# Optimization experiments

Hardware: AMD Instinct MI355X
Metric: run time of the kernel (lower is better)

## Reference

```python
import jax, jax.numpy as jnp
import numpy as np

WIN, SHIFT = 8, 4
DIM, HEADS, MLP_H = 96, 6, 384
B, H, W = 1, 512, 512
HEAD_D = DIM // HEADS
N = WIN * WIN
EPS = 1e-5


def _rel_pos_index():
    ch = np.arange(WIN)
    coords = np.stack(np.meshgrid(ch, ch, indexing='ij')).reshape(2, -1)  # [2, 64]
    rel = (coords[:, :, None] - coords[:, None, :]).transpose(1, 2, 0)    # [64, 64, 2]
    rel[:, :, 0] += WIN - 1
    rel[:, :, 1] += WIN - 1
    rel[:, :, 0] *= 2 * WIN - 1
    return rel.sum(-1)


def _attn_mask():
    img = np.zeros((H, W))
    cnt = 0
    for hs in (slice(0, -WIN), slice(-WIN, -SHIFT), slice(-SHIFT, None)):
        for ws in (slice(0, -WIN), slice(-WIN, -SHIFT), slice(-SHIFT, None)):
            img[hs, ws] = cnt
            cnt += 1
    mw = img.reshape(H // WIN, WIN, W // WIN, WIN).transpose(0, 2, 1, 3).reshape(-1, N)
    diff = mw[:, None, :] - mw[:, :, None]
    return np.where(diff != 0, -100.0, 0.0).astype(np.float32)  # [nW, 64, 64]


REL_IDX = jnp.asarray(_rel_pos_index())
ATTN_MASK = jnp.asarray(_attn_mask())


def layernorm(x, w, b):
    mu = jnp.mean(x, axis=-1, keepdims=True)
    var = jnp.mean(jnp.square(x - mu), axis=-1, keepdims=True)
    return (x - mu) * jax.lax.rsqrt(var + EPS) * w + b


def setup_inputs() -> dict:
    key = jax.random.key(0)
    ks = jax.random.split(key, 16)
    s = 0.02
    return {
        'x': jax.random.normal(ks[0], (B, DIM, H, W), jnp.float32),
        'norm1_w': jnp.ones((DIM,), jnp.float32),
        'norm1_b': jnp.zeros((DIM,), jnp.float32),
        'qkv_w': jax.random.normal(ks[1], (3 * DIM, DIM), jnp.float32) * s,
        'qkv_b': jnp.zeros((3 * DIM,), jnp.float32),
        'rpb': jax.random.normal(ks[2], ((2 * WIN - 1) ** 2, HEADS), jnp.float32) * s,
        'proj_w': jax.random.normal(ks[3], (DIM, DIM), jnp.float32) * s,
        'proj_b': jnp.zeros((DIM,), jnp.float32),
        'norm2_w': jnp.ones((DIM,), jnp.float32),
        'norm2_b': jnp.zeros((DIM,), jnp.float32),
        'fc1_w': jax.random.normal(ks[4], (MLP_H, DIM), jnp.float32) * s,
        'fc1_b': jnp.zeros((MLP_H,), jnp.float32),
        'fc2_w': jax.random.normal(ks[5], (DIM, MLP_H), jnp.float32) * s,
        'fc2_b': jnp.zeros((DIM,), jnp.float32),
    }


def reference(x, norm1_w, norm1_b, qkv_w, qkv_b, rpb, proj_w, proj_b,
              norm2_w, norm2_b, fc1_w, fc1_b, fc2_w, fc2_b):
    nH, nW_ = H // WIN, W // WIN
    nWin = nH * nW_
    shortcut = jnp.transpose(x, (0, 2, 3, 1))            # [B,H,W,C]
    xn = layernorm(shortcut, norm1_w, norm1_b)
    xs = jnp.roll(xn, (-SHIFT, -SHIFT), axis=(1, 2))     # cyclic shift
    # window partition -> [B*nWin, N, C]
    win = xs.reshape(B, nH, WIN, nW_, WIN, DIM).transpose(0, 1, 3, 2, 4, 5)
    win = win.reshape(B * nWin, N, DIM)
    qkv = win @ qkv_w.T + qkv_b                          # [Bw, N, 3C]
    qkv = qkv.reshape(-1, N, 3, HEADS, HEAD_D).transpose(2, 0, 3, 1, 4)
    q, k, v = qkv[0], qkv[1], qkv[2]                     # [Bw, h, N, d]
    scale = HEAD_D ** -0.5
    attn = jnp.einsum('bhnd,bhmd->bhnm', q * scale, k)   # [Bw, h, 64, 64]
    bias = rpb[REL_IDX.reshape(-1)].reshape(N, N, HEADS).transpose(2, 0, 1)
    attn = attn + bias[None]
    attn = attn.reshape(B, nWin, HEADS, N, N) + ATTN_MASK[None, :, None]
    attn = jax.nn.softmax(attn.reshape(-1, HEADS, N, N), axis=-1)
    out = jnp.einsum('bhnm,bhmd->bhnd', attn, v).transpose(0, 2, 1, 3).reshape(-1, N, DIM)
    out = out @ proj_w.T + proj_b
    # window reverse + un-shift
    out = out.reshape(B, nH, nW_, WIN, WIN, DIM).transpose(0, 1, 3, 2, 4, 5).reshape(B, H, W, DIM)
    out = jnp.roll(out, (SHIFT, SHIFT), axis=(1, 2))
    x1 = shortcut + out
    h = layernorm(x1, norm2_w, norm2_b)
    h = jax.nn.gelu(h @ fc1_w.T + fc1_b, approximate=False) @ fc2_w.T + fc2_b
    x2 = x1 + h
    return jnp.transpose(x2, (0, 3, 1, 2))               # [B,C,H,W]
```

## Files before the change

kernel.cpp:

```cpp
#include <hip/hip_runtime.h>
#include <math.h>

#define WINSZ  8
#define SHIFTV 4
#define DIM    96
#define HEADS  6
#define HEAD_D 16
#define MLP_H  384
#define HH     512
#define WWID   512
#define HWSZ   (HH*WWID)
#define NTOK   64
#define EPSV   1e-5f
#define XP     97
#define QP     17
#define BFP    120

#define OFF_W1   0
#define OFF_W2   36864
#define OFF_QKV  73728
#define OFF_PROJ 101376
#define OFF_BIAS 110592
#define WS_FULL  208896
#define WS_MLP   73728

#define QKP 104
#define VTP 72
#define X1P 97
#define WBP 104

#define WBUF_OFF 38144
#define SMEM_SZ  48128

typedef __attribute__((ext_vector_type(2))) short  s2v;
typedef __attribute__((ext_vector_type(4))) short  s4v;
typedef __attribute__((ext_vector_type(8))) short  s8v;
typedef __attribute__((ext_vector_type(4))) float  f4v;
typedef __attribute__((ext_vector_type(4))) unsigned short u4v;

__device__ __forceinline__ unsigned short f2bf(float v) {
    union { float f; unsigned u; } c; c.f = v;
    unsigned r = c.u + 0x7fffu + ((c.u >> 16) & 1u);
    return (unsigned short)(r >> 16);
}
__device__ __forceinline__ float bf2f(unsigned short u) {
    union { unsigned u; float f; } c; c.u = ((unsigned)u) << 16; return c.f;
}
__device__ __forceinline__ unsigned long long shfl64(unsigned long long v, int src) {
    union { unsigned long long q; int i[2]; } c; c.q = v;
    c.i[0] = __shfl(c.i[0], src);
    c.i[1] = __shfl(c.i[1], src);
    return c.q;
}
__device__ __forceinline__ float fast_gelu(float h) {
    float h2 = h*h;
    float u  = fmaf(0.044715f, h2, 1.0f);
    float e  = __expf(-1.5957691216057308f * h * u);
    return h * __builtin_amdgcn_rcpf(1.0f + e);
}

__device__ __forceinline__ void gld_lds16(const void* g, void* l) {
    __builtin_amdgcn_global_load_lds(
        (const __attribute__((address_space(1))) unsigned*)(g),
        (__attribute__((address_space(3))) unsigned*)(l),
        16, 0, 0);
}

__device__ __forceinline__ void stage48(const char* gb, int stride_b,
                                        char* wb, int tid) {
    #pragma unroll
    for (int k = 0; k < 3; ++k) {
        int idx = tid + k*256;
        if (k < 2 || idx < 624) {
            int r   = idx / 13;
            int rem = idx - r*13;
            const char* src = (rem < 12) ? (gb + r*stride_b + rem*16) : gb;
            char* dst = wb + ((tid & ~63) + k*256)*16;
            gld_lds16(src, dst);
        }
    }
}

__global__ __launch_bounds__(256) void conv_all(
    const float* __restrict__ qkvw, const float* __restrict__ projw,
    const float* __restrict__ f1w,  const float* __restrict__ f2w,
    const float* __restrict__ rpb,  short* __restrict__ ws)
{
    int i = blockIdx.x*256 + threadIdx.x;
    if (i < 36864)        ws[OFF_W1 + i] = (short)f2bf(f1w[i]);
    else if (i < 73728)   ws[OFF_W2 + i-36864] = (short)f2bf(f2w[i-36864]);
    else if (i < 101376)  ws[OFF_QKV + i-73728] = (short)f2bf(qkvw[i-73728]);
    else if (i < 110592)  ws[OFF_PROJ + i-101376] = (short)f2bf(projw[i-101376]);
    else if (i < WS_FULL) {
        int idx = i - 110592;
        int tb = idx / 24576;
        int rm = idx - tb*24576;
        int hd = rm >> 12;
        int rc = rm & 4095;
        int r = rc >> 6, c = rc & 63;
        int rti = r>>3, rtj = r&7, cti = c>>3, ctj = c&7;
        int rel = (rti-cti+7)*15 + (rtj-ctj+7);
        float b = rpb[rel*HEADS + hd];
        int bh = tb>>1, bw = tb&1;
        int rhr = bh ? (rti<4?1:2) : 0, rhc = bh ? (cti<4?1:2) : 0;
        int rwr = bw ? (rtj<4?1:2) : 0, rwc = bw ? (ctj<4?1:2) : 0;
        if (rhr != rhc || rwr != rwc) b -= 100.f;
        ws[OFF_BIAS + idx] = (short)f2bf(b);
    }
}

__global__ __launch_bounds__(256,3) void fused_kernel(
    const float* __restrict__ x,
    const float* __restrict__ n1w, const float* __restrict__ n1b,
    const float* __restrict__ qkvb, const float* __restrict__ projb,
    const float* __restrict__ n2w, const float* __restrict__ n2b,
    const float* __restrict__ f1b, const float* __restrict__ f2b,
    const short* __restrict__ wqkv, const short* __restrict__ wproj,
    const short* __restrict__ w1b, const short* __restrict__ w2b,
    const short* __restrict__ btab,
    float* __restrict__ out)
{
    __shared__ __align__(16) char smem[SMEM_SZ];
    short* qb   = (short*)smem;
    short* kb2  = (short*)(smem + 13312);
    short* vT   = (short*)(smem + 26624);
    short* aob  = qb;
    float* x1f  = (float*)(smem + 13312);
    short* lnb2 = (short*)smem;
    short* hid  = (short*)smem;
    short* wbS  = (short*)(smem + WBUF_OFF);
    char*  wbC  = (char*)(smem + WBUF_OFF);

    const int tid  = threadIdx.x;
    const int wv   = tid >> 6, lane = tid & 63;
    const int col  = lane & 15, kq = lane >> 4;
    const int trow = wv*16 + col;

    int bid = blockIdx.x;
    int wl = (bid & 7)*512 + ((bid >> 5) << 2) + ((bid >> 3) & 3);
    const int wi = wl >> 6, wj = wl & 63;

    const int ti = trow>>3, tj = trow&7;
    const int hpos = (wi*8 + ti + SHIFTV) & (HH-1);
    const int wpos = (wj*8 + tj + SHIFTV) & (WWID-1);
    const int p = hpos*WWID + wpos;

    s8v bfr[3];
    {
        float v[24], s1 = 0.f, s2 = 0.f;
        #pragma unroll
        for (int kb = 0; kb < 3; ++kb)
            #pragma unroll
            for (int j = 0; j < 8; ++j) {
                float vv = x[(kb*32 + kq*8 + j)*HWSZ + p];
                v[kb*8+j] = vv; s1 += vv; s2 += vv*vv;
            }
        s1 += __shfl_xor(s1, 16); s2 += __shfl_xor(s2, 16);
        s1 += __shfl_xor(s1, 32); s2 += __shfl_xor(s2, 32);
        float mu = s1*(1.f/96.f);
        float rs = rsqrtf(s2*(1.f/96.f) - mu*mu + EPSV);
        #pragma unroll
        for (int kb = 0; kb < 3; ++kb) {
            f4v wA = *(const f4v*)&n1w[kb*32 + kq*8];
            f4v wB = *(const f4v*)&n1w[kb*32 + kq*8 + 4];
            f4v bA = *(const f4v*)&n1b[kb*32 + kq*8];
            f4v bB = *(const f4v*)&n1b[kb*32 + kq*8 + 4];
            s8v o;
            #pragma unroll
            for (int j = 0; j < 4; ++j) {
                o[j]   = (short)f2bf((v[kb*8+j]  -mu)*rs*wA[j] + bA[j]);
                o[4+j] = (short)f2bf((v[kb*8+4+j]-mu)*rs*wB[j] + bB[j]);
            }
            bfr[kb] = o;
        }
    }

    float shc[24];
    #pragma unroll
    for (int mt = 0; mt < 6; ++mt)
        #pragma unroll
        for (int i = 0; i < 4; ++i)
            shc[mt*4+i] = x[(mt*16 + kq*4 + i)*HWSZ + p];

    const s8v zfrag = {0,0,0,0,0,0,0,0};

    {
        #pragma unroll
        for (int g = 0; g < 6; ++g) {
            s8v aw[9];
            #pragma unroll
            for (int m = 0; m < 3; ++m)
                #pragma unroll
                for (int kb = 0; kb < 3; ++kb)
                    aw[m*3+kb] = *(const s8v*)&wqkv[((g*3+m)*16+col)*96 + kb*32 + kq*8];
            #pragma unroll
            for (int m = 0; m < 3; ++m) {
                int mt = g*3 + m;
                f4v acc = {0.f,0.f,0.f,0.f};
                #pragma unroll
                for (int kb = 0; kb < 3; ++kb)
                    acc = __builtin_amdgcn_mfma_f32_16x16x32_bf16(aw[m*3+kb], bfr[kb], acc, 0,0,0);
                int od0 = mt*16 + kq*4;
                f4v bia = *(const f4v*)&qkvb[od0];
                if (mt < 6) {
                    s4v o;
                    #pragma unroll
                    for (int i = 0; i < 4; ++i) o[i] = (short)f2bf((acc[i]+bia[i])*0.25f);
                    *(s4v*)&qb[trow*QKP + od0] = o;
                } else if (mt < 12) {
                    s4v o;
                    #pragma unroll
                    for (int i = 0; i < 4; ++i) o[i] = (short)f2bf(acc[i]+bia[i]);
                    *(s4v*)&kb2[trow*QKP + od0 - 96] = o;
                } else {
                    int d0 = od0 - 192;
                    #pragma unroll
                    for (int i = 0; i < 4; ++i)
                        vT[(d0+i)*VTP + trow] = (short)f2bf(acc[i]+bia[i]);
                }
            }
        }
    }
    __syncthreads();

    const int tb = ((wi==63)?2:0) | ((wj==63)?1:0);
    u4v bt[4];
    {
        const short* gb = btab + ((tb*6+0)<<12) + (trow<<6);
        #pragma unroll
        for (int mt = 0; mt < 4; ++mt) bt[mt] = *(const u4v*)&gb[mt*16 + kq*4];
    }
    for (int hd = 0; hd < 6; ++hd) {
        u4v btn[4];
        if (hd < 5) {
            const short* gb = btab + ((tb*6+hd+1)<<12) + (trow<<6);
            #pragma unroll
            for (int mt = 0; mt < 4; ++mt) btn[mt] = *(const u4v*)&gb[mt*16 + kq*4];
        }
        s8v bq = zfrag;
        if (kq < 2) bq = *(const s8v*)&qb[trow*QKP + hd*16 + kq*8];
        f4v st[4];
        #pragma unroll
        for (int mt = 0; mt < 4; ++mt) {
            s8v a = zfrag;
            if (kq < 2) a = *(const s8v*)&kb2[(mt*16+col)*QKP + hd*16 + kq*8];
            f4v z = {0.f,0.f,0.f,0.f};
            st[mt] = __builtin_amdgcn_mfma_f32_16x16x32_bf16(a, bq, z, 0,0,0);
        }
        float sc[16];
        #pragma unroll
        for (int mt = 0; mt < 4; ++mt) {
            #pragma unroll
            for (int i = 0; i < 4; ++i) sc[mt*4+i] = st[mt][i] + bf2f(bt[mt][i]);
        }
        float m8[8];
        #pragma unroll
        for (int j = 0; j < 8; ++j) m8[j] = fmaxf(sc[2*j], sc[2*j+1]);
        #pragma unroll
        for (int j = 0; j < 4; ++j) m8[j] = fmaxf(m8[j], m8[j+4]);
        float m = fmaxf(fmaxf(m8[0], m8[2]), fmaxf(m8[1], m8[3]));
        m = fmaxf(m, __shfl_xor(m, 16));
        m = fmaxf(m, __shfl_xor(m, 32));
        float s8r[8];
        #pragma unroll
        for (int j = 0; j < 8; ++j) {
            sc[2*j]   = __expf(sc[2*j]  -m);
            sc[2*j+1] = __expf(sc[2*j+1]-m);
            s8r[j] = sc[2*j] + sc[2*j+1];
        }
        #pragma unroll
        for (int j = 0; j < 4; ++j) s8r[j] += s8r[j+4];
        float sum = (s8r[0]+s8r[2]) + (s8r[1]+s8r[3]);
        sum += __shfl_xor(sum, 16);
        sum += __shfl_xor(sum, 32);
        unsigned long long p64[4];
        #pragma unroll
        for (int mt = 0; mt < 4; ++mt) {
            union { s4v v; unsigned long long q; } pk;
            #pragma unroll
            for (int i = 0; i < 4; ++i) pk.v[i] = (short)f2bf(sc[mt*4+i]);
            p64[mt] = pk.q;
        }
        const int s0 = col + ((kq & 1) << 5);
        const int sel = kq >> 1;
        f4v g = {0.f,0.f,0.f,0.f};
        #pragma unroll
        for (int c = 0; c < 2; ++c) {
            unsigned long long t0 = shfl64(p64[2*c],   s0);
            unsigned long long t1 = shfl64(p64[2*c+1], s0);
            unsigned long long lo = sel ? t1 : t0;
            unsigned long long u0 = shfl64(p64[2*c],   s0+16);
            unsigned long long u1 = shfl64(p64[2*c+1], s0+16);
            unsigned long long hi = sel ? u1 : u0;
            union { unsigned long long q[2]; s8v v; } bb;
            bb.q[0] = lo; bb.q[1] = hi;
            s8v a = *(const s8v*)&vT[(hd*16+col)*VTP + c*32 + kq*8];
            g = __builtin_amdgcn_mfma_f32_16x16x32_bf16(a, bb.v, g, 0,0,0);
        }
        float linv = 1.f/sum;
        s4v o;
        #pragma unroll
        for (int i = 0; i < 4; ++i) o[i] = (short)f2bf(g[i]*linv);
        *(s4v*)&aob[trow*QKP + hd*16 + kq*4] = o;
        #pragma unroll
        for (int mt = 0; mt < 4; ++mt) bt[mt] = btn[mt];
    }
    __syncthreads();

    stage48((const char*)w1b, 192, wbC, tid);

    {
        s8v bfr2[3];
        #pragma unroll
        for (int kb = 0; kb < 3; ++kb)
            bfr2[kb] = *(const s8v*)&aob[trow*QKP + kb*32 + kq*8];
        #pragma unroll
        for (int g = 0; g < 2; ++g) {
            s8v aw[9];
            #pragma unroll
            for (int m = 0; m < 3; ++m)
                #pragma unroll
                for (int kb = 0; kb < 3; ++kb)
                    aw[m*3+kb] = *(const s8v*)&wproj[((g*3+m)*16+col)*96 + kb*32 + kq*8];
            #pragma unroll
            for (int m = 0; m < 3; ++m) {
                int mt = g*3 + m;
                f4v acc = {0.f,0.f,0.f,0.f};
                #pragma unroll
                for (int kb = 0; kb < 3; ++kb)
                    acc = __builtin_amdgcn_mfma_f32_16x16x32_bf16(aw[m*3+kb], bfr2[kb], acc, 0,0,0);
                int c0 = mt*16 + kq*4;
                f4v pb4 = *(const f4v*)&projb[c0];
                #pragma unroll
                for (int i = 0; i < 4; ++i)
                    x1f[trow*X1P + c0 + i] = shc[mt*4+i] + acc[i] + pb4[i];
            }
        }
    }
    __threadfence_block();

    const int mrow = wv*16;

    {
        int t2 = mrow + col;
        float vv[24], s1 = 0.f, s2 = 0.f;
        #pragma unroll
        for (int i = 0; i < 24; ++i) {
            float v = x1f[t2*X1P + kq*24 + i]; vv[i] = v; s1 += v; s2 += v*v;
        }
        s1 += __shfl_xor(s1, 16); s2 += __shfl_xor(s2, 16);
        s1 += __shfl_xor(s1, 32); s2 += __shfl_xor(s2, 32);
        float mu = s1*(1.f/96.f);
        float rs = rsqrtf(s2*(1.f/96.f) - mu*mu + EPSV);
        #pragma unroll
        for (int i = 0; i < 12; ++i) {
            int c = kq*24 + i*2;
            s2v o;
            o[0] = (short)f2bf((vv[i*2]  -mu)*rs*n2w[c]   + n2b[c]);
            o[1] = (short)f2bf((vv[i*2+1]-mu)*rs*n2w[c+1] + n2b[c+1]);
            *(s2v*)&lnb2[t2*QKP + c] = o;
        }
    }
    __threadfence_block();

    s8v a1[3];
    #pragma unroll
    for (int kb = 0; kb < 3; ++kb)
        a1[kb] = *(const s8v*)&lnb2[(mrow+col)*QKP + kb*32 + kq*8];

    f4v acc2[6];
    #pragma unroll
    for (int n = 0; n < 6; ++n) acc2[n] = (f4v){0.f,0.f,0.f,0.f};

    __syncthreads();

    for (int ch = 0; ch < 4; ++ch) {
        const char* w1c = (const char*)w1b + ch*96*192;
        const char* w2c = (const char*)w2b + ch*192;
        #pragma unroll
        for (int half = 0; half < 2; ++half) {
            #pragma unroll
            for (int nl = 0; nl < 3; ++nl) {
                f4v acc = (f4v){0.f,0.f,0.f,0.f};
                #pragma unroll
                for (int kb = 0; kb < 3; ++kb) {
                    s8v b = *(const s8v*)&wbS[(nl*16+col)*WBP + kb*32 + kq*8];
                    acc = __builtin_amdgcn_mfma_f32_16x16x32_bf16(a1[kb], b, acc, 0,0,0);
                }
                int c = half*48 + nl*16 + col;
                float bias = f1b[ch*96 + c];
                #pragma unroll
                for (int i = 0; i < 4; ++i)
                    hid[(mrow + kq*4 + i)*QKP + c] = (short)f2bf(fast_gelu(acc[i]+bias));
            }
            __syncthreads();
            if (half == 0) stage48(w1c + 48*192, 192, wbC, tid);
            else           stage48(w2c, 768, wbC, tid);
            __syncthreads();
        }
        s8v a2[3];
        #pragma unroll
        for (int kb = 0; kb < 3; ++kb)
            a2[kb] = *(const s8v*)&hid[(mrow+col)*QKP + kb*32 + kq*8];
        #pragma unroll
        for (int half = 0; half < 2; ++half) {
            #pragma unroll
            for (int nl = 0; nl < 3; ++nl) {
                #pragma unroll
                for (int kb = 0; kb < 3; ++kb) {
                    s8v b = *(const s8v*)&wbS[(nl*16+col)*WBP + kb*32 + kq*8];
                    acc2[half*3+nl] = __builtin_amdgcn_mfma_f32_16x16x32_bf16(a2[kb], b, acc2[half*3+nl], 0,0,0);
                }
            }
            __syncthreads();
            if (half == 0)      stage48(w2c + 48*768, 768, wbC, tid);
            else if (ch < 3)    stage48((const char*)w1b + (ch+1)*96*192, 192, wbC, tid);
            __syncthreads();
        }
    }

    #pragma unroll
    for (int nt = 0; nt < 6; ++nt) {
        int c = nt*16 + col;
        float bias = f2b[c];
        #pragma unroll
        for (int i = 0; i < 4; ++i) {
            int t = mrow + kq*4 + i;
            x1f[t*X1P + c] += acc2[nt][i] + bias;
        }
    }
    __threadfence_block();
    {
        int tt = mrow + col;
        int tti = tt>>3, ttj = tt&7;
        int pp = ((wi*8 + tti + SHIFTV) & (HH-1))*WWID + ((wj*8 + ttj + SHIFTV) & (WWID-1));
        #pragma unroll
        for (int it = 0; it < 24; ++it) {
            int c = it*4 + kq;
            out[c*HWSZ + pp] = x1f[tt*X1P + c];
        }
    }
}

__global__ __launch_bounds__(256) void attn_kernel(
    const float* __restrict__ x,
    const float* __restrict__ n1w, const float* __restrict__ n1b,
    const float* __restrict__ qkvw, const float* __restrict__ qkvb,
    const float* __restrict__ rpb,
    const float* __restrict__ projw, const float* __restrict__ projb,
    float* __restrict__ out)
{
    __shared__ float xn[NTOK*XP];
    __shared__ float ao[NTOK*XP];
    __shared__ float qh[NTOK*QP];
    __shared__ float kh[NTOK*QP];
    __shared__ float vh[NTOK*QP];
    __shared__ int   srid[NTOK];
    __shared__ int   spos[NTOK];

    const int tid = threadIdx.x;
    const int blk = blockIdx.x;
    const int wi = blk >> 6, wj = blk & 63;

    {
        int t  = tid >> 2;
        int j4 = tid & 3;
        int ti = t >> 3, tj = t & 7;
        int a = wi*WINSZ + ti;
        int bcol = wj*WINSZ + tj;
        int h = (a + SHIFTV) & (HH-1);
        int w = (bcol + SHIFTV) & (WWID-1);
        int p = h*WWID + w;
        if (j4 == 0) {
            spos[t] = p;
            int rh = (a < HH-WINSZ) ? 0 : (a < HH-SHIFTV ? 1 : 2);
            int rw = (bcol < WWID-WINSZ) ? 0 : (bcol < WWID-SHIFTV ? 1 : 2);
            srid[t] = rh*3 + rw;
        }
        float xv[24];
        float s1 = 0.f, s2 = 0.f;
        int c0 = j4*24;
        #pragma unroll
        for (int i = 0; i < 24; ++i) {
            float v = x[(c0+i)*HWSZ + p];
            xv[i] = v; s1 += v; s2 += v*v;
        }
        s1 += __shfl_xor(s1,1); s2 += __shfl_xor(s2,1);
        s1 += __shfl_xor(s1,2); s2 += __shfl_xor(s2,2);
        float mu  = s1 * (1.f/96.f);
        float var = s2 * (1.f/96.f) - mu*mu;
        float rs  = rsqrtf(var + EPSV);
        #pragma unroll
        for (int i = 0; i < 24; ++i) {
            int c = c0 + i;
            xn[t*XP + c] = (xv[i]-mu)*rs*n1w[c] + n1b[c];
        }
    }
    __syncthreads();

    const int wv   = tid >> 6;
    const int lane = tid & 63;
    const int r    = tid >> 2;
    const int g    = tid & 3;
    const int rti  = r >> 3, rtj = r & 7;

    for (int hd = 0; hd < HEADS; ++hd) {
        for (int it = 0; it < 12; ++it) {
            int ol = it*4 + wv;
            int s = ol >> 4, d = ol & 15;
            int grow = __builtin_amdgcn_readfirstlane(s*DIM + hd*HEAD_D + d);
            const float* wr = qkvw + grow*DIM;
            float acc = qkvb[grow];
            #pragma unroll 8
            for (int c = 0; c < DIM; ++c)
                acc = fmaf(xn[lane*XP+c], wr[c], acc);
            float* dst = (s==0) ? qh : ((s==1) ? kh : vh);
            dst[lane*QP + d] = acc;
        }
        __syncthreads();

        float qr[16];
        #pragma unroll
        for (int d = 0; d < 16; ++d) qr[d] = qh[r*QP+d];
        float scr[16];
        int myrid = srid[r];
        #pragma unroll
        for (int jj = 0; jj < 16; ++jj) {
            int colx = g*16 + jj;
            float a = 0.f;
            #pragma unroll
            for (int d = 0; d < 16; ++d) a = fmaf(qr[d], kh[colx*QP+d], a);
            int cti = colx >> 3, ctj = colx & 7;
            int rel = (rti - cti + 7)*15 + (rtj - ctj + 7);
            float b = rpb[rel*HEADS + hd];
            float m = (srid[colx]==myrid) ? 0.f : -100.f;
            scr[jj] = a*0.25f + b + m;
        }
        float mx = scr[0];
        #pragma unroll
        for (int jj = 1; jj < 16; ++jj) mx = fmaxf(mx, scr[jj]);
        mx = fmaxf(mx, __shfl_xor(mx,1));
        mx = fmaxf(mx, __shfl_xor(mx,2));
        float sum = 0.f;
        #pragma unroll
        for (int jj = 0; jj < 16; ++jj) { scr[jj] = __expf(scr[jj]-mx); sum += scr[jj]; }
        sum += __shfl_xor(sum,1);
        sum += __shfl_xor(sum,2);
        float inv = 1.f/sum;
        #pragma unroll
        for (int d = 0; d < 16; ++d) {
            float a = 0.f;
            #pragma unroll
            for (int jj = 0; jj < 16; ++jj) a = fmaf(scr[jj], vh[(g*16+jj)*QP+d], a);
            a += __shfl_xor(a,1);
            a += __shfl_xor(a,2);
            if (g == 0) ao[r*XP + hd*HEAD_D + d] = a*inv;
        }
        __syncthreads();
    }

    for (int it = 0; it < 24; ++it) {
        int c = __builtin_amdgcn_readfirstlane(it*4 + wv);
        const float* wr = projw + c*DIM;
        float acc = projb[c];
        #pragma unroll 8
        for (int k = 0; k < DIM; ++k)
            acc = fmaf(ao[lane*XP+k], wr[k], acc);
        int p2 = spos[lane];
        float shc = x[c*HWSZ + p2];
        out[c*HWSZ + p2] = shc + acc;
    }
}

__global__ __launch_bounds__(256) void mlp_mfma(
    float* __restrict__ io,
    const float* __restrict__ n2w, const float* __restrict__ n2b,
    const short* __restrict__ w1b, const float* __restrict__ f1b,
    const short* __restrict__ w2b, const float* __restrict__ f2b)
{
    __shared__ short lnbuf[64*BFP];
    __shared__ __align__(16) char ubuf[64*XP*4];
    float* lnf = (float*)ubuf;
    short* hbc = (short*)ubuf;

    const int tid  = threadIdx.x;
    const int base = blockIdx.x * 64;

    for (int idx = tid; idx < 64*DIM; idx += 256) {
        int c = idx >> 6, t = idx & 63;
        lnf[t*XP + c] = io[c*HWSZ + base + t];
    }
    __syncthreads();
    {
        int t = tid >> 2, q = tid & 3;
        float xv[24], s1 = 0.f, s2 = 0.f;
        #pragma unroll
        for (int i = 0; i < 24; ++i) {
            float v = lnf[t*XP + q*24 + i]; xv[i] = v; s1 += v; s2 += v*v;
        }
        s1 += __shfl_xor(s1,1); s2 += __shfl_xor(s2,1);
        s1 += __shfl_xor(s1,2); s2 += __shfl_xor(s2,2);
        float mu = s1*(1.f/96.f);
        float rs = rsqrtf(s2*(1.f/96.f) - mu*mu + EPSV);
        #pragma unroll
        for (int i = 0; i < 24; ++i) {
            int c = q*24 + i;
            lnbuf[t*BFP + c] = (short)f2bf((xv[i]-mu)*rs*n2w[c] + n2b[c]);
        }
    }
    __syncthreads();

    const int l = tid & 63, wv = tid >> 6;
    const int mrow = wv*16;
    const int col = l & 15, kq = l >> 4;

    s8v a1[3];
    #pragma unroll
    for (int kb = 0; kb < 3; ++kb)
        a1[kb] = *(const s8v*)&lnbuf[(mrow+col)*BFP + kb*32 + kq*8];

    f4v acc2[6];
    #pragma unroll
    for (int n = 0; n < 6; ++n) acc2[n] = (f4v){0.f,0.f,0.f,0.f};

    for (int ch = 0; ch < 4; ++ch) {
        #pragma unroll
        for (int nt = 0; nt < 6; ++nt) {
            int n0 = ch*96 + nt*16;
            f4v acc = (f4v){0.f,0.f,0.f,0.f};
            #pragma unroll
            for (int kb = 0; kb < 3; ++kb) {
                s8v b = *(const s8v*)&w1b[(n0+col)*96 + kb*32 + kq*8];
                acc = __builtin_amdgcn_mfma_f32_16x16x32_bf16(a1[kb], b, acc, 0, 0, 0);
            }
            float bias = f1b[n0+col];
            #pragma unroll
            for (int i = 0; i < 4; ++i) {
                float g = fast_gelu(acc[i] + bias);
                hbc[(mrow + kq*4 + i)*BFP + nt*16 + col] = (short)f2bf(g);
            }
        }
        __threadfence_block();
        s8v a2[3];
        #pragma unroll
        for (int kb = 0; kb < 3; ++kb)
            a2[kb] = *(const s8v*)&hbc[(mrow+col)*BFP + kb*32 + kq*8];
        #pragma unroll
        for (int nt = 0; nt < 6; ++nt) {
            #pragma unroll
            for (int kb = 0; kb < 3; ++kb) {
                s8v b = *(const s8v*)&w2b[(nt*16+col)*MLP_H + ch*96 + kb*32 + kq*8];
                acc2[nt] = __builtin_amdgcn_mfma_f32_16x16x32_bf16(a2[kb], b, acc2[nt], 0, 0, 0);
            }
        }
        __threadfence_block();
    }

    #pragma unroll
    for (int nt = 0; nt < 6; ++nt) {
        int c = nt*16 + col;
        float bias = f2b[c];
        #pragma unroll
        for (int i = 0; i < 4; ++i) {
            int t = mrow + kq*4 + i;
            float* p = &io[c*HWSZ + base + t];
            *p = *p + acc2[nt][i] + bias;
        }
    }
}

__global__ __launch_bounds__(256) void conv_w(
    const float* __restrict__ f1w, const float* __restrict__ f2w,
    short* __restrict__ ws)
{
    int i = blockIdx.x*256 + threadIdx.x;
    if (i < 36864)      ws[i] = (short)f2bf(f1w[i]);
    else if (i < 73728) ws[i] = (short)f2bf(f2w[i-36864]);
}

extern "C" void kernel_launch(void* const* d_in, const int* in_sizes, int n_in,
                              void* d_out, int out_size, void* d_ws, size_t ws_size,
                              hipStream_t stream) {
    const float* x     = (const float*)d_in[0];
    const float* n1w   = (const float*)d_in[1];
    const float* n1b   = (const float*)d_in[2];
    const float* qkvw  = (const float*)d_in[3];
    const float* qkvb  = (const float*)d_in[4];
    const float* rpb   = (const float*)d_in[5];
    const float* projw = (const float*)d_in[6];
    const float* projb = (const float*)d_in[7];
    const float* n2w   = (const float*)d_in[8];
    const float* n2b   = (const float*)d_in[9];
    const float* f1w   = (const float*)d_in[10];
    const float* f1b   = (const float*)d_in[11];
    const float* f2w   = (const float*)d_in[12];
    const float* f2b   = (const float*)d_in[13];
    float* out = (float*)d_out;

    if (ws_size >= (size_t)WS_FULL * sizeof(short)) {
        short* wsb = (short*)d_ws;
        hipLaunchKernelGGL(conv_all, dim3(816), dim3(256), 0, stream,
                           qkvw, projw, f1w, f2w, rpb, wsb);
        hipLaunchKernelGGL(fused_kernel, dim3(4096), dim3(256), 0, stream,
                           x, n1w, n1b, qkvb, projb, n2w, n2b, f1b, f2b,
                           wsb + OFF_QKV, wsb + OFF_PROJ,
                           wsb + OFF_W1, wsb + OFF_W2, wsb + OFF_BIAS, out);
    } else {
        short* wsb = (short*)d_ws;
        hipLaunchKernelGGL(attn_kernel, dim3(4096), dim3(256), 0, stream,
                           x, n1w, n1b, qkvw, qkvb, rpb, projw, projb, out);
        hipLaunchKernelGGL(conv_w, dim3(288), dim3(256), 0, stream, f1w, f2w, wsb);
        hipLaunchKernelGGL(mlp_mfma, dim3(4096), dim3(256), 0, stream,
                           out, n2w, n2b, wsb, f1b, wsb + 36864, f2b);
    }
}
```

Baseline: 395.9 us.

## Double-buffer MLP weight staging, keep x1 in registers, raise occupancy

The fused kernel now stages MLP weight chunks into two LDS buffers. Each chunk is prefetched two steps ahead, which removes one barrier per step and overlaps the global-to-LDS copies with MFMA work. The residual x1 stays in registers through LayerNorm2 and the MLP instead of going through a shared float buffer. That shrinks LDS use enough to raise launch bounds from 3 to 4 blocks per CU. The weight conversion kernel is also vectorized to 4 elements per thread; the risk is extra register pressure or spills from the 24 live floats.

```diff
diff --git a/kernel.cpp b/kernel.cpp
--- a/kernel.cpp
+++ b/kernel.cpp
@@ -29,8 +29,9 @@
 #define X1P 97
 #define WBP 104
 
-#define WBUF_OFF 38144
-#define SMEM_SZ  48128
+#define WBA_OFF 13312
+#define WBB_OFF 23296
+#define SMEM_SZ 40448
 
 typedef __attribute__((ext_vector_type(2))) short  s2v;
 typedef __attribute__((ext_vector_type(4))) short  s4v;
@@ -81,35 +82,62 @@
     }
 }
 
+__device__ __forceinline__ void stage_chunk(const char* w1B, const char* w2B,
+                                            int n, char* dst, int tid) {
+    int ch = n >> 2, s = n & 3;
+    const char* src; int stride;
+    if      (s == 0) { src = w1B + ch*96*192;            stride = 192; }
+    else if (s == 1) { src = w1B + ch*96*192 + 48*192;   stride = 192; }
+    else if (s == 2) { src = w2B + ch*192;               stride = 768; }
+    else             { src = w2B + ch*192 + 48*768;      stride = 768; }
+    stage48(src, stride, dst, tid);
+}
+
 __global__ __launch_bounds__(256) void conv_all(
     const float* __restrict__ qkvw, const float* __restrict__ projw,
     const float* __restrict__ f1w,  const float* __restrict__ f2w,
     const float* __restrict__ rpb,  short* __restrict__ ws)
 {
-    int i = blockIdx.x*256 + threadIdx.x;
-    if (i < 36864)        ws[OFF_W1 + i] = (short)f2bf(f1w[i]);
-    else if (i < 73728)   ws[OFF_W2 + i-36864] = (short)f2bf(f2w[i-36864]);
-    else if (i < 101376)  ws[OFF_QKV + i-73728] = (short)f2bf(qkvw[i-73728]);
-    else if (i < 110592)  ws[OFF_PROJ + i-101376] = (short)f2bf(projw[i-101376]);
-    else if (i < WS_FULL) {
+    int i = (blockIdx.x*256 + threadIdx.x)*4;
+    if (i < 110592) {
+        const float* src; int off;
+        if (i < 36864)       { src = f1w;  off = i;          }
+        else if (i < 73728)  { src = f2w;  off = i - 36864;  }
+        else if (i < 101376) { src = qkvw; off = i - 73728;  }
+        else                 { src = projw; off = i - 101376; }
+        f4v v = *(const f4v*)&src[off];
+        s4v o;
+        #pragma unroll
+        for (int j = 0; j < 4; ++j) o[j] = (short)f2bf(v[j]);
+        *(s4v*)&ws[i] = o;
+    } else if (i < WS_FULL) {
         int idx = i - 110592;
         int tb = idx / 24576;
         int rm = idx - tb*24576;
         int hd = rm >> 12;
         int rc = rm & 4095;
-        int r = rc >> 6, c = rc & 63;
-        int rti = r>>3, rtj = r&7, cti = c>>3, ctj = c&7;
-        int rel = (rti-cti+7)*15 + (rtj-ctj+7);
-        float b = rpb[rel*HEADS + hd];
+        int r = rc >> 6, c0 = rc & 63;
+        int rti = r>>3, rtj = r&7;
         int bh = tb>>1, bw = tb&1;
-        int rhr = bh ? (rti<4?1:2) : 0, rhc = bh ? (cti<4?1:2) : 0;
-        int rwr = bw ? (rtj<4?1:2) : 0, rwc = bw ? (ctj<4?1:2) : 0;
-        if (rhr != rhc || rwr != rwc) b -= 100.f;
-        ws[OFF_BIAS + idx] = (short)f2bf(b);
-    }
-}
-
-__global__ __launch_bounds__(256,3) void fused_kernel(
+        int rhr = bh ? (rti<4?1:2) : 0;
+        int rwr = bw ? (rtj<4?1:2) : 0;
+        s4v o;
+        #pragma unroll
+        for (int j = 0; j < 4; ++j) {
+            int c = c0 + j;
+            int cti = c>>3, ctj = c&7;
+            int rel = (rti-cti+7)*15 + (rtj-ctj+7);
+            float b = rpb[rel*HEADS + hd];
+            int rhc = bh ? (cti<4?1:2) : 0;
+            int rwc = bw ? (ctj<4?1:2) : 0;
+            if (rhr != rhc || rwr != rwc) b -= 100.f;
+            o[j] = (short)f2bf(b);
+        }
+        *(s4v*)&ws[OFF_BIAS + idx] = o;
+    }
+}
+
+__global__ __launch_bounds__(256,4) void fused_kernel(
     const float* __restrict__ x,
     const float* __restrict__ n1w, const float* __restrict__ n1b,
     const float* __restrict__ qkvb, const float* __restrict__ projb,
@@ -125,11 +153,11 @@
     short* kb2  = (short*)(smem + 13312);
     short* vT   = (short*)(smem + 26624);
     short* aob  = qb;
-    float* x1f  = (float*)(smem + 13312);
     short* lnb2 = (short*)smem;
     short* hid  = (short*)smem;
-    short* wbS  = (short*)(smem + WBUF_OFF);
-    char*  wbC  = (char*)(smem + WBUF_OFF);
+    short* wbA  = (short*)(smem + WBA_OFF);
+    short* wbB  = (short*)(smem + WBB_OFF);
+    float* x1f  = (float*)smem;
 
     const int tid  = threadIdx.x;
     const int wv   = tid >> 6, lane = tid & 63;
@@ -307,8 +335,10 @@
     }
     __syncthreads();
 
-    stage48((const char*)w1b, 192, wbC, tid);
-
+    stage_chunk((const char*)w1b, (const char*)w2b, 0, (char*)wbA, tid);
+    stage_chunk((const char*)w1b, (const char*)w2b, 1, (char*)wbB, tid);
+
+    float x1r[24];
     {
         s8v bfr2[3];
         #pragma unroll
@@ -333,32 +363,31 @@
                 f4v pb4 = *(const f4v*)&projb[c0];
                 #pragma unroll
                 for (int i = 0; i < 4; ++i)
-                    x1f[trow*X1P + c0 + i] = shc[mt*4+i] + acc[i] + pb4[i];
-            }
-        }
-    }
-    __threadfence_block();
+                    x1r[mt*4+i] = shc[mt*4+i] + acc[i] + pb4[i];
+            }
+        }
+    }
 
     const int mrow = wv*16;
 
     {
-        int t2 = mrow + col;
-        float vv[24], s1 = 0.f, s2 = 0.f;
-        #pragma unroll
-        for (int i = 0; i < 24; ++i) {
-            float v = x1f[t2*X1P + kq*24 + i]; vv[i] = v; s1 += v; s2 += v*v;
-        }
+        float s1 = 0.f, s2 = 0.f;
+        #pragma unroll
+        for (int j = 0; j < 24; ++j) { s1 += x1r[j]; s2 += x1r[j]*x1r[j]; }
         s1 += __shfl_xor(s1, 16); s2 += __shfl_xor(s2, 16);
         s1 += __shfl_xor(s1, 32); s2 += __shfl_xor(s2, 32);
         float mu = s1*(1.f/96.f);
         float rs = rsqrtf(s2*(1.f/96.f) - mu*mu + EPSV);
         #pragma unroll
-        for (int i = 0; i < 12; ++i) {
-            int c = kq*24 + i*2;
-            s2v o;
-            o[0] = (short)f2bf((vv[i*2]  -mu)*rs*n2w[c]   + n2b[c]);
-            o[1] = (short)f2bf((vv[i*2+1]-mu)*rs*n2w[c+1] + n2b[c+1]);
-            *(s2v*)&lnb2[t2*QKP + c] = o;
+        for (int mt = 0; mt < 6; ++mt) {
+            int c0 = mt*16 + kq*4;
+            f4v w4 = *(const f4v*)&n2w[c0];
+            f4v b4 = *(const f4v*)&n2b[c0];
+            s4v o;
+            #pragma unroll
+            for (int i = 0; i < 4; ++i)
+                o[i] = (short)f2bf((x1r[mt*4+i]-mu)*rs*w4[i] + b4[i]);
+            *(s4v*)&lnb2[trow*QKP + c0] = o;
         }
     }
     __threadfence_block();
@@ -374,51 +403,62 @@
 
     __syncthreads();
 
+    #pragma unroll
     for (int ch = 0; ch < 4; ++ch) {
-        const char* w1c = (const char*)w1b + ch*96*192;
-        const char* w2c = (const char*)w2b + ch*192;
-        #pragma unroll
-        for (int half = 0; half < 2; ++half) {
+        #pragma unroll
+        for (int sub = 0; sub < 2; ++sub) {
+            const int cidx = ch*4 + sub;
+            const short* wb = (cidx & 1) ? wbB : wbA;
             #pragma unroll
             for (int nl = 0; nl < 3; ++nl) {
                 f4v acc = (f4v){0.f,0.f,0.f,0.f};
                 #pragma unroll
                 for (int kb = 0; kb < 3; ++kb) {
-                    s8v b = *(const s8v*)&wbS[(nl*16+col)*WBP + kb*32 + kq*8];
+                    s8v b = *(const s8v*)&wb[(nl*16+col)*WBP + kb*32 + kq*8];
                     acc = __builtin_amdgcn_mfma_f32_16x16x32_bf16(a1[kb], b, acc, 0,0,0);
                 }
-                int c = half*48 + nl*16 + col;
-                float bias = f1b[ch*96 + c];
+                int cch = sub*48 + nl*16 + col;
+                float bias = f1b[ch*96 + cch];
                 #pragma unroll
                 for (int i = 0; i < 4; ++i)
-                    hid[(mrow + kq*4 + i)*QKP + c] = (short)f2bf(fast_gelu(acc[i]+bias));
+                    hid[(mrow + kq*4 + i)*QKP + cch] = (short)f2bf(fast_gelu(acc[i]+bias));
             }
             __syncthreads();
-            if (half == 0) stage48(w1c + 48*192, 192, wbC, tid);
-            else           stage48(w2c, 768, wbC, tid);
-            __syncthreads();
+            if (cidx + 2 < 16)
+                stage_chunk((const char*)w1b, (const char*)w2b, cidx+2,
+                            (char*)((cidx & 1) ? wbB : wbA), tid);
         }
         s8v a2[3];
         #pragma unroll
         for (int kb = 0; kb < 3; ++kb)
             a2[kb] = *(const s8v*)&hid[(mrow+col)*QKP + kb*32 + kq*8];
         #pragma unroll
-        for (int half = 0; half < 2; ++half) {
+        for (int sub = 0; sub < 2; ++sub) {
+            const int cidx = ch*4 + 2 + sub;
+            const short* wb = (cidx & 1) ? wbB : wbA;
             #pragma unroll
             for (int nl = 0; nl < 3; ++nl) {
+                int nt = sub*3 + nl;
                 #pragma unroll
                 for (int kb = 0; kb < 3; ++kb) {
-                    s8v b = *(const s8v*)&wbS[(nl*16+col)*WBP + kb*32 + kq*8];
-                    acc2[half*3+nl] = __builtin_amdgcn_mfma_f32_16x16x32_bf16(a2[kb], b, acc2[half*3+nl], 0,0,0);
+                    s8v b = *(const s8v*)&wb[(nl*16+col)*WBP + kb*32 + kq*8];
+                    acc2[nt] = __builtin_amdgcn_mfma_f32_16x16x32_bf16(a2[kb], b, acc2[nt], 0,0,0);
                 }
             }
             __syncthreads();
-            if (half == 0)      stage48(w2c + 48*768, 768, wbC, tid);
-            else if (ch < 3)    stage48((const char*)w1b + (ch+1)*96*192, 192, wbC, tid);
-            __syncthreads();
-        }
-    }
-
+            if (cidx + 2 < 16)
+                stage_chunk((const char*)w1b, (const char*)w2b, cidx+2,
+                            (char*)((cidx & 1) ? wbB : wbA), tid);
+        }
+    }
+
+    #pragma unroll
+    for (int mt = 0; mt < 6; ++mt) {
+        #pragma unroll
+        for (int i = 0; i < 4; ++i)
+            x1f[trow*X1P + mt*16 + kq*4 + i] = x1r[mt*4+i];
+    }
+    __threadfence_block();
     #pragma unroll
     for (int nt = 0; nt < 6; ++nt) {
         int c = nt*16 + col;
@@ -699,7 +739,7 @@
 
     if (ws_size >= (size_t)WS_FULL * sizeof(short)) {
         short* wsb = (short*)d_ws;
-        hipLaunchKernelGGL(conv_all, dim3(816), dim3(256), 0, stream,
+        hipLaunchKernelGGL(conv_all, dim3(204), dim3(256), 0, stream,
                            qkvw, projw, f1w, f2w, rpb, wsb);
         hipLaunchKernelGGL(fused_kernel, dim3(4096), dim3(256), 0, stream,
                            x, n1w, n1b, qkvb, projb, n2w, n2b, f1b, f2b,
```

Result: no change. 400.4 us (+1.1%).
